# Kernel tuning notes

Hardware: AMD Instinct MI355X
Metric: run time of the kernel (lower is better)

## Reference

```python
import jax, jax.numpy as jnp
import numpy as np

H = 768
HEADS = 12
HD = H // HEADS
INTER = 3072
EPS = 1e-6


def setup_inputs() -> dict:
    key = jax.random.key(0)
    ks = jax.random.split(key, 10)
    B, T = 4, 1024
    scale = 0.02
    return {
        "x": jax.random.normal(ks[0], (B, T, H), jnp.float32),
        "mask": jnp.ones((B, T), jnp.float32),
        "w_qkv": jax.random.normal(ks[1], (H, 3 * H), jnp.float32) * scale,
        "w_o": jax.random.normal(ks[2], (H, H), jnp.float32) * scale,
        "tau": jnp.full((HEADS,), 5.0, jnp.float32),
        "w1": jax.random.normal(ks[3], (H, INTER), jnp.float32) * scale,
        "b1": jnp.zeros((INTER,), jnp.float32),
        "w2": jax.random.normal(ks[4], (INTER, H), jnp.float32) * scale,
        "b2": jnp.zeros((H,), jnp.float32),
        "nb1": jnp.zeros((H,), jnp.float32),
        "nb2": jnp.zeros((H,), jnp.float32),
    }


def _block(x, mask, w_qkv, w_o, tau, w1, b1, w2, b2, nb1, nb2):
    B, T, C = x.shape
    qkv = x @ w_qkv                                  # [B,T,3H]
    q, k, v = jnp.split(qkv, 3, axis=-1)
    q = q.reshape(B, T, HEADS, HD)
    k = k.reshape(B, T, HEADS, HD)
    v = v.reshape(B, T, HEADS, HD)
    # 2quad attention: quadratic-normalized scores instead of softmax
    s = jnp.einsum("bthd,bshd->bhts", q, k) / jnp.sqrt(jnp.float32(HD))
    s = s / tau[None, :, None, None]
    w = s * s                                        # [B,HEADS,T,T]
    w = w * mask[:, None, None, :]                   # zero masked keys
    w = w / (jnp.sum(w, axis=-1, keepdims=True) + EPS)
    out = jnp.einsum("bhts,bshd->bthd", w, v).reshape(B, T, C)
    out = out @ w_o
    x = x + 0.2 * out + nb1                          # scaled residual + bias-only norm1
    ffn = jax.nn.relu(x @ w1 + b1) @ w2 + b2
    x = x + ffn + nb2                                # residual + bias-only norm2
    return x


def reference(x, mask, w_qkv, w_o, tau, w1, b1, w2, b2, nb1, nb2):
    return _block(x, mask, w_qkv, w_o, tau, w1, b1, w2, b2, nb1, nb2)
```

## Files before the change

### kernel.cpp

```cpp
#include <hip/hip_runtime.h>

typedef __bf16 bf16x8 __attribute__((ext_vector_type(8)));
typedef float f32x4 __attribute__((ext_vector_type(4)));
typedef unsigned short u16;
typedef unsigned long long u64;

#define HDIM 768
#define NHEADS 12
#define SEQ 1024
#define NBATCH 4
#define ROWS 4096
#define QKV3 2304
#define INTERDIM 3072

__device__ __forceinline__ u16 f2bf(float f) {
  union { float f; unsigned int u; } v; v.f = f;
  unsigned int r = v.u + 0x7fffu + ((v.u >> 16) & 1u);
  return (u16)(r >> 16);
}

__device__ __forceinline__ void gload16(const u16* g, u16* l) {
  __builtin_amdgcn_global_load_lds(
      (const __attribute__((address_space(1))) void*)g,
      (__attribute__((address_space(3))) void*)l, 16, 0, 0);
}

__device__ __forceinline__ unsigned ldsoff(const void* p) {
  return (unsigned)(unsigned long long)(const __attribute__((address_space(3))) char*)p;
}

__device__ __forceinline__ u64 tr8(unsigned a) {
  u64 r;
  asm volatile("ds_read_b64_tr_b16 %0, %1" : "=v"(r) : "v"(a));
  return r;
}

union B8 { u64 q[2]; bf16x8 v; };

__global__ __launch_bounds__(256) void k_prep(
    const float* __restrict__ x, u16* __restrict__ xb,
    const float* __restrict__ wqkv, u16* __restrict__ wqkvT,
    const float* __restrict__ wo, u16* __restrict__ woT,
    const float* __restrict__ w1, u16* __restrict__ w1T,
    const float* __restrict__ w2, u16* __restrict__ w2T) {
  __shared__ float tile[32][33];
  int bid = blockIdx.x, tid = threadIdx.x;
  if (bid < 3072) {
    int i = bid * 256 + tid;
    float4 f = reinterpret_cast<const float4*>(x)[i];
    ushort4 o;
    o.x = f2bf(f.x); o.y = f2bf(f.y); o.z = f2bf(f.z); o.w = f2bf(f.w);
    reinterpret_cast<ushort4*>(xb)[i] = o;
    return;
  }
  const float* in; u16* outp; int K, N, t;
  if (bid < 4800)      { in = wqkv; outp = wqkvT; K = 768;  N = 2304; t = bid - 3072; }
  else if (bid < 5376) { in = wo;   outp = woT;   K = 768;  N = 768;  t = bid - 4800; }
  else if (bid < 7680) { in = w1;   outp = w1T;   K = 768;  N = 3072; t = bid - 5376; }
  else                 { in = w2;   outp = w2T;   K = 3072; N = 768;  t = bid - 7680; }
  int ntx = N >> 5;
  int bx = t % ntx, by = t / ntx;
  int tx = tid & 31, ty = tid >> 5;
  int n0 = bx * 32, k0 = by * 32;
#pragma unroll
  for (int i = 0; i < 32; i += 8)
    tile[ty + i][tx] = in[(size_t)(k0 + ty + i) * N + n0 + tx];
  __syncthreads();
#pragma unroll
  for (int i = 0; i < 32; i += 8)
    outp[(size_t)(n0 + ty + i) * K + k0 + tx] = f2bf(tile[tx][ty + i]);
}

template<int BN, int MODE>
__global__ __launch_bounds__(256) void k_gemm(
    const u16* __restrict__ A, const u16* __restrict__ Bt,
    int M, int N, int K, int ksplit,
    u16* __restrict__ obf, float* __restrict__ of32,
    const float* __restrict__ e1, const float* __restrict__ e2) {
  constexpr int BM = 128, BK = 64;
  constexpr int WC = (BN == 128) ? 2 : 1;
  constexpr int WR = 4 / WC;
  constexpr int WM = BM / WR;
  constexpr int WN = BN / WC;
  constexpr int MFR = WM / 16;
  constexpr int NFR = WN / 16;
  constexpr int AISS = BM / 32;
  constexpr int BISS = BN / 32;
  __shared__ u16 As[BM * BK];
  __shared__ u16 Bs[BN * BK];
  int tid = threadIdx.x, lane = tid & 63, wid = tid >> 6;
  int wr = wid / WC, wc = wid % WC;

  int gx = gridDim.x;
  int nwg = gx * gridDim.y;
  int orig = blockIdx.y * gx + blockIdx.x;
  int cpx = nwg >> 3;
  int swz = (orig & 7) * cpx + (orig >> 3);
  int bx = swz % gx, by = swz / gx;

  int m0 = by * BM, n0 = bx * BN;
  int Kc = K / ksplit, k0 = blockIdx.z * Kc;
  int fr = lane & 15, fg = lane >> 4, fk = fg * 8;

  f32x4 acc[MFR][NFR] = {};

  int r = tid >> 3;
  int cswz = ((tid & 7) * 8) ^ ((r & 3) << 4);
  const u16* Ag = A + (size_t)(m0 + r) * K + k0 + cswz;
  const u16* Bg = Bt + (size_t)(n0 + r) * K + k0 + cswz;
  u16* Asl = &As[wid * 512];
  u16* Bsl = &Bs[wid * 512];

  for (int kt = 0; kt < Kc; kt += BK) {
    __syncthreads();
#pragma unroll
    for (int i = 0; i < AISS; i++)
      gload16(Ag + kt + (size_t)(i * 32) * K, Asl + i * 2048);
#pragma unroll
    for (int i = 0; i < BISS; i++)
      gload16(Bg + kt + (size_t)(i * 32) * K, Bsl + i * 2048);
    __syncthreads();

#pragma unroll
    for (int kk = 0; kk < 2; kk++) {
      bf16x8 af[MFR], bfv[NFR];
#pragma unroll
      for (int mi = 0; mi < MFR; mi++) {
        int row = wr * WM + mi * 16 + fr;
        int ce = (kk * 32 + fk) ^ ((row & 3) << 4);
        af[mi] = *reinterpret_cast<const bf16x8*>(&As[row * BK + ce]);
      }
#pragma unroll
      for (int ni = 0; ni < NFR; ni++) {
        int row = wc * WN + ni * 16 + fr;
        int ce = (kk * 32 + fk) ^ ((row & 3) << 4);
        bfv[ni] = *reinterpret_cast<const bf16x8*>(&Bs[row * BK + ce]);
      }
#pragma unroll
      for (int mi = 0; mi < MFR; mi++)
#pragma unroll
        for (int ni = 0; ni < NFR; ni++)
          acc[mi][ni] = __builtin_amdgcn_mfma_f32_16x16x32_bf16(af[mi], bfv[ni], acc[mi][ni], 0, 0, 0);
    }
  }

  float* part = (MODE == 3) ? of32 + (size_t)blockIdx.z * ((size_t)M * N) : of32;
#pragma unroll
  for (int mi = 0; mi < MFR; mi++) {
#pragma unroll
    for (int ni = 0; ni < NFR; ni++) {
#pragma unroll
      for (int i = 0; i < 4; i++) {
        int row = m0 + wr * WM + mi * 16 + fg * 4 + i;
        int col = n0 + wc * WN + ni * 16 + fr;
        float v = acc[mi][ni][i];
        size_t idx = (size_t)row * N + col;
        if constexpr (MODE == 0) {
          obf[idx] = f2bf(v);
        } else if constexpr (MODE == 1) {
          float t = e1[idx] + 0.2f * v + e2[col];
          of32[idx] = t;
          obf[idx] = f2bf(t);
        } else if constexpr (MODE == 2) {
          float t = v + e1[col];
          t = t > 0.f ? t : 0.f;
          obf[idx] = f2bf(t);
        } else {
          part[idx] = v;
        }
      }
    }
  }
}

__global__ void k_ffn2_reduce(const float* __restrict__ p, const float* __restrict__ x1f,
                              const float* __restrict__ b2, const float* __restrict__ nb2,
                              float* __restrict__ out) {
  int i = blockIdx.x * 256 + threadIdx.x;
  int col4 = (i * 4) % HDIM;
  float4 s = reinterpret_cast<const float4*>(x1f)[i];
  float4 bb = *reinterpret_cast<const float4*>(b2 + col4);
  float4 nn = *reinterpret_cast<const float4*>(nb2 + col4);
  s.x += bb.x + nn.x; s.y += bb.y + nn.y; s.z += bb.z + nn.z; s.w += bb.w + nn.w;
#pragma unroll
  for (int z = 0; z < 2; z++) {
    float4 pv = reinterpret_cast<const float4*>(p + (size_t)z * ROWS * HDIM)[i];
    s.x += pv.x; s.y += pv.y; s.z += pv.z; s.w += pv.w;
  }
  reinterpret_cast<float4*>(out)[i] = s;
}

__global__ __launch_bounds__(512) void k_attn(
    const u16* __restrict__ qkv, const float* __restrict__ mask,
    const float* __restrict__ tau, u16* __restrict__ outp) {
  __shared__ u16 Ks[64 * 72];
  __shared__ u16 Vs[64 * 64];
  __shared__ u16 Ps[8 * 1024];
  int tid = threadIdx.x, lane = tid & 63, w = tid >> 6;
  int h = blockIdx.y, b = blockIdx.z;
  int fr = lane & 15, fg = lane >> 4, fk = fg * 8;
  int rb = b * SEQ;
  float rs = 1.0f / (8.0f * tau[h]);
  float rs2 = rs * rs;

  int t0 = blockIdx.x * 128 + w * 16;
  const u16* qrow = qkv + (size_t)(rb + t0 + fr) * QKV3 + h * 64;
  bf16x8 aq0 = *reinterpret_cast<const bf16x8*>(qrow + fk);
  bf16x8 aq1 = *reinterpret_cast<const bf16x8*>(qrow + 32 + fk);

  f32x4 acco[4] = {};
  f32x4 accd = {};

  int sr = tid >> 3, c = tid & 7;
  const u16* kg = qkv + (size_t)(rb + sr) * QKV3 + HDIM + h * 64 + c * 8;
  const u16* vg = kg + HDIM;
  u16* kw = &Ks[sr * 72 + c * 8];
  u16* vw = &Vs[((sr >> 2) * 4 + (c >> 1)) * 64 + (sr & 3) * 16 + (c & 1) * 8];
  unsigned psb = ldsoff(&Ps[w * 1024]);
  unsigned vsb = ldsoff(Vs);

  __bf16 onev = (__bf16)1.0f;
  bf16x8 ones = {onev, onev, onev, onev, onev, onev, onev, onev};

  int4 kreg = *reinterpret_cast<const int4*>(kg);
  int4 vreg = *reinterpret_cast<const int4*>(vg);

  for (int st = 0; st < SEQ; st += 64) {
    __syncthreads();
    *reinterpret_cast<int4*>(kw) = kreg;
    *reinterpret_cast<int4*>(vw) = vreg;
    __syncthreads();
    if (st + 64 < SEQ) {
      kreg = *reinterpret_cast<const int4*>(kg + (size_t)(st + 64) * QKV3);
      vreg = *reinterpret_cast<const int4*>(vg + (size_t)(st + 64) * QKV3);
    }

#pragma unroll
    for (int sf = 0; sf < 4; sf++) {
      bf16x8 bk0 = *reinterpret_cast<const bf16x8*>(&Ks[(sf * 16 + fr) * 72 + fk]);
      bf16x8 bk1 = *reinterpret_cast<const bf16x8*>(&Ks[(sf * 16 + fr) * 72 + 32 + fk]);
      f32x4 s = {};
      s = __builtin_amdgcn_mfma_f32_16x16x32_bf16(aq0, bk0, s, 0, 0, 0);
      s = __builtin_amdgcn_mfma_f32_16x16x32_bf16(aq1, bk1, s, 0, 0, 0);
      float rm = rs2 * mask[b * SEQ + st + sf * 16 + fr];
      u64 pw = 0;
#pragma unroll
      for (int i = 0; i < 4; i++) {
        float wv = s[i] * s[i] * rm;
        pw |= (u64)f2bf(wv) << (16 * i);
      }
      *reinterpret_cast<u64*>(&Ps[w * 1024 + (sf * 4 + (fr >> 2)) * 64 + (fr & 3) * 16 + fg * 4]) = pw;
    }
    asm volatile("s_waitcnt lgkmcnt(0)" ::: "memory");
    __builtin_amdgcn_sched_barrier(0);

    u64 pa0 = tr8(psb + (fg * 2 + 0) * 128 + fr * 2);
    u64 pa1 = tr8(psb + (fg * 2 + 1) * 128 + fr * 2);
    u64 pa2 = tr8(psb + (8 + fg * 2 + 0) * 128 + fr * 2);
    u64 pa3 = tr8(psb + (8 + fg * 2 + 1) * 128 + fr * 2);
    u64 vb[4][4];
#pragma unroll
    for (int df = 0; df < 4; df++) {
      vb[df][0] = tr8(vsb + ((fg * 2 + 0) * 4 + df) * 128 + fr * 2);
      vb[df][1] = tr8(vsb + ((fg * 2 + 1) * 4 + df) * 128 + fr * 2);
      vb[df][2] = tr8(vsb + ((8 + fg * 2 + 0) * 4 + df) * 128 + fr * 2);
      vb[df][3] = tr8(vsb + ((8 + fg * 2 + 1) * 4 + df) * 128 + fr * 2);
    }
    asm volatile("s_waitcnt lgkmcnt(0)" ::: "memory");
    __builtin_amdgcn_sched_barrier(0);

    B8 ap0, ap1;
    ap0.q[0] = pa0; ap0.q[1] = pa1;
    ap1.q[0] = pa2; ap1.q[1] = pa3;
#pragma unroll
    for (int df = 0; df < 4; df++) {
      B8 b0, b1;
      b0.q[0] = vb[df][0]; b0.q[1] = vb[df][1];
      b1.q[0] = vb[df][2]; b1.q[1] = vb[df][3];
      acco[df] = __builtin_amdgcn_mfma_f32_16x16x32_bf16(ap0.v, b0.v, acco[df], 0, 0, 0);
      acco[df] = __builtin_amdgcn_mfma_f32_16x16x32_bf16(ap1.v, b1.v, acco[df], 0, 0, 0);
    }
    accd = __builtin_amdgcn_mfma_f32_16x16x32_bf16(ap0.v, ones, accd, 0, 0, 0);
    accd = __builtin_amdgcn_mfma_f32_16x16x32_bf16(ap1.v, ones, accd, 0, 0, 0);
  }

#pragma unroll
  for (int df = 0; df < 4; df++)
#pragma unroll
    for (int i = 0; i < 4; i++) {
      int t = t0 + fg * 4 + i;
      int col = h * 64 + df * 16 + fr;
      float o = acco[df][i] / (accd[i] + 1e-6f);
      outp[(size_t)(rb + t) * HDIM + col] = f2bf(o);
    }
}

extern "C" void kernel_launch(void* const* d_in, const int* in_sizes, int n_in,
                              void* d_out, int out_size, void* d_ws, size_t ws_size,
                              hipStream_t stream) {
  const float* x     = (const float*)d_in[0];
  const float* mask  = (const float*)d_in[1];
  const float* w_qkv = (const float*)d_in[2];
  const float* w_o   = (const float*)d_in[3];
  const float* tau   = (const float*)d_in[4];
  const float* w1    = (const float*)d_in[5];
  const float* b1    = (const float*)d_in[6];
  const float* w2    = (const float*)d_in[7];
  const float* b2    = (const float*)d_in[8];
  const float* nb1   = (const float*)d_in[9];
  const float* nb2   = (const float*)d_in[10];
  float* out = (float*)d_out;
  (void)ws_size; (void)in_sizes; (void)n_in; (void)out_size;

  char* base = (char*)d_ws;
  float* part = (float*)base;
  u16* xb    = (u16*)(base);
  u16* wqkvT = (u16*)(base + 6291456);
  u16* woT   = (u16*)(base + 9830400);
  u16* w1T   = (u16*)(base + 11010048);
  u16* qkvb  = (u16*)(base + 15728640);
  u16* attnb = (u16*)(base + 34603008);
  u16* x1b   = (u16*)(base + 40894464);
  u16* w2T   = (u16*)(base + 50331648);
  float* x1f = (float*)(base + 55050240);
  u16* hb    = (u16*)(base + 67633152);

  k_prep<<<9984, 256, 0, stream>>>(x, xb, w_qkv, wqkvT, w_o, woT, w1, w1T, w2, w2T);

  k_gemm<128, 0><<<dim3(QKV3 / 128, ROWS / 128), 256, 0, stream>>>(
      xb, wqkvT, ROWS, QKV3, HDIM, 1, qkvb, nullptr, nullptr, nullptr);
  k_attn<<<dim3(SEQ / 128, NHEADS, NBATCH), 512, 0, stream>>>(qkvb, mask, tau, attnb);
  k_gemm<64, 1><<<dim3(HDIM / 64, ROWS / 128), 256, 0, stream>>>(
      attnb, woT, ROWS, HDIM, HDIM, 1, x1b, x1f, x, nb1);
  k_gemm<128, 2><<<dim3(INTERDIM / 128, ROWS / 128), 256, 0, stream>>>(
      x1b, w1T, ROWS, INTERDIM, HDIM, 1, hb, nullptr, b1, nullptr);
  k_gemm<64, 3><<<dim3(HDIM / 64, ROWS / 128, 2), 256, 0, stream>>>(
      hb, w2T, ROWS, HDIM, INTERDIM, 2, nullptr, part, nullptr, nullptr);
  k_ffn2_reduce<<<ROWS * HDIM / 4 / 256, 256, 0, stream>>>(part, x1f, b2, nb2, out);
}
```

Before: 164.6 us.

## Use 256x256 double-buffered 8-wave GEMM with split-K 4 for FFN2

Replaces the 128-wide GEMM for the QKV, FFN1 and FFN2 projections with a 256x256-tile, 512-thread kernel. It double-buffers LDS, prefetches the next A and B k-tiles between MFMA phases, and raises wave priority during MFMA bursts. The aim is more data reuse per tile and overlap of global loads with matrix math. FFN2 moves to split-K 4 with a wider partial reduction, and the output projection keeps a dedicated 128x64 kernel. The trade-off is far fewer workgroups than the 256 CUs (144–192 blocks), large LDS use (128KB per block), more partial-sum traffic, and a larger workspace overlapping earlier buffers.

```diff
diff --git a/kernel.cpp b/kernel.cpp
--- a/kernel.cpp
+++ b/kernel.cpp
@@ -71,103 +71,236 @@
     outp[(size_t)(n0 + ty + i) * K + k0 + tx] = f2bf(tile[tx][ty + i]);
 }
 
-template<int BN, int MODE>
-__global__ __launch_bounds__(256) void k_gemm(
+template<int MODE>
+__global__ __launch_bounds__(512, 2) void k_gemm256(
     const u16* __restrict__ A, const u16* __restrict__ Bt,
     int M, int N, int K, int ksplit,
     u16* __restrict__ obf, float* __restrict__ of32,
-    const float* __restrict__ e1, const float* __restrict__ e2) {
-  constexpr int BM = 128, BK = 64;
-  constexpr int WC = (BN == 128) ? 2 : 1;
-  constexpr int WR = 4 / WC;
-  constexpr int WM = BM / WR;
-  constexpr int WN = BN / WC;
-  constexpr int MFR = WM / 16;
-  constexpr int NFR = WN / 16;
-  constexpr int AISS = BM / 32;
-  constexpr int BISS = BN / 32;
-  __shared__ u16 As[BM * BK];
-  __shared__ u16 Bs[BN * BK];
+    const float* __restrict__ e1) {
+  __shared__ u16 lds[2][2][256 * 64];
   int tid = threadIdx.x, lane = tid & 63, wid = tid >> 6;
-  int wr = wid / WC, wc = wid % WC;
+  int wr = wid >> 2, wc = wid & 3;
+  int fr = lane & 15, fg = lane >> 4, fk = fg * 8;
 
   int gx = gridDim.x;
   int nwg = gx * gridDim.y;
   int orig = blockIdx.y * gx + blockIdx.x;
-  int cpx = nwg >> 3;
-  int swz = (orig & 7) * cpx + (orig >> 3);
+  int swz = (orig & 7) * (nwg >> 3) + (orig >> 3);
   int bx = swz % gx, by = swz / gx;
-
-  int m0 = by * BM, n0 = bx * BN;
+  int m0 = by * 256, n0 = bx * 256;
   int Kc = K / ksplit, k0 = blockIdx.z * Kc;
-  int fr = lane & 15, fg = lane >> 4, fk = fg * 8;
-
-  f32x4 acc[MFR][NFR] = {};
+
+  f32x4 acc[8][4] = {};
 
   int r = tid >> 3;
   int cswz = ((tid & 7) * 8) ^ ((r & 3) << 4);
   const u16* Ag = A + (size_t)(m0 + r) * K + k0 + cswz;
   const u16* Bg = Bt + (size_t)(n0 + r) * K + k0 + cswz;
-  u16* Asl = &As[wid * 512];
-  u16* Bsl = &Bs[wid * 512];
-
-  for (int kt = 0; kt < Kc; kt += BK) {
-    __syncthreads();
-#pragma unroll
-    for (int i = 0; i < AISS; i++)
-      gload16(Ag + kt + (size_t)(i * 32) * K, Asl + i * 2048);
-#pragma unroll
-    for (int i = 0; i < BISS; i++)
-      gload16(Bg + kt + (size_t)(i * 32) * K, Bsl + i * 2048);
-    __syncthreads();
-
-#pragma unroll
-    for (int kk = 0; kk < 2; kk++) {
-      bf16x8 af[MFR], bfv[NFR];
-#pragma unroll
-      for (int mi = 0; mi < MFR; mi++) {
-        int row = wr * WM + mi * 16 + fr;
-        int ce = (kk * 32 + fk) ^ ((row & 3) << 4);
-        af[mi] = *reinterpret_cast<const bf16x8*>(&As[row * BK + ce]);
-      }
-#pragma unroll
-      for (int ni = 0; ni < NFR; ni++) {
-        int row = wc * WN + ni * 16 + fr;
-        int ce = (kk * 32 + fk) ^ ((row & 3) << 4);
-        bfv[ni] = *reinterpret_cast<const bf16x8*>(&Bs[row * BK + ce]);
-      }
-#pragma unroll
-      for (int mi = 0; mi < MFR; mi++)
-#pragma unroll
-        for (int ni = 0; ni < NFR; ni++)
-          acc[mi][ni] = __builtin_amdgcn_mfma_f32_16x16x32_bf16(af[mi], bfv[ni], acc[mi][ni], 0, 0, 0);
-    }
-  }
+
+#define STAGE_A(buf, kt) do {                                        \
+    u16* d_ = &lds[buf][0][wid * 512];                               \
+    _Pragma("unroll")                                                \
+    for (int i_ = 0; i_ < 4; i_++)                                   \
+      gload16(Ag + (kt) + (size_t)(i_ * 64) * K, d_ + i_ * 4096);    \
+  } while (0)
+#define STAGE_B(buf, kt) do {                                        \
+    u16* d_ = &lds[buf][1][wid * 512];                               \
+    _Pragma("unroll")                                                \
+    for (int i_ = 0; i_ < 4; i_++)                                   \
+      gload16(Bg + (kt) + (size_t)(i_ * 64) * K, d_ + i_ * 4096);    \
+  } while (0)
+
+  int sw = (fr & 3) << 4;
+  int ce0 = fk ^ sw, ce1 = (32 + fk) ^ sw;
+
+  STAGE_A(0, 0);
+  STAGE_B(0, 0);
+  asm volatile("s_waitcnt vmcnt(0)" ::: "memory");
+  __builtin_amdgcn_s_barrier();
+
+  int nt = Kc / 64;
+  bf16x8 af[4][2], bv0[2][2], bv1[2][2];
+  for (int t = 0; t < nt; t++) {
+    int cur = t & 1;
+    const u16* Ab = &lds[cur][0][0];
+    const u16* Bb = &lds[cur][1][0];
+    bool pf = (t + 1 < nt);
+
+    if (pf) STAGE_A(cur ^ 1, (t + 1) * 64);
+#pragma unroll
+    for (int im = 0; im < 4; im++) {
+      int row = wr * 128 + im * 16 + fr;
+      af[im][0] = *reinterpret_cast<const bf16x8*>(&Ab[row * 64 + ce0]);
+      af[im][1] = *reinterpret_cast<const bf16x8*>(&Ab[row * 64 + ce1]);
+    }
+#pragma unroll
+    for (int in = 0; in < 2; in++) {
+      int row = wc * 64 + in * 16 + fr;
+      bv0[in][0] = *reinterpret_cast<const bf16x8*>(&Bb[row * 64 + ce0]);
+      bv0[in][1] = *reinterpret_cast<const bf16x8*>(&Bb[row * 64 + ce1]);
+    }
+    __builtin_amdgcn_s_barrier();
+    __builtin_amdgcn_s_setprio(1);
+#pragma unroll
+    for (int im = 0; im < 4; im++)
+#pragma unroll
+      for (int in = 0; in < 2; in++)
+#pragma unroll
+        for (int kk = 0; kk < 2; kk++)
+          acc[im][in] = __builtin_amdgcn_mfma_f32_16x16x32_bf16(af[im][kk], bv0[in][kk], acc[im][in], 0, 0, 0);
+    __builtin_amdgcn_s_setprio(0);
+    __builtin_amdgcn_s_barrier();
+
+    if (pf) STAGE_B(cur ^ 1, (t + 1) * 64);
+#pragma unroll
+    for (int in = 0; in < 2; in++) {
+      int row = wc * 64 + (2 + in) * 16 + fr;
+      bv1[in][0] = *reinterpret_cast<const bf16x8*>(&Bb[row * 64 + ce0]);
+      bv1[in][1] = *reinterpret_cast<const bf16x8*>(&Bb[row * 64 + ce1]);
+    }
+    __builtin_amdgcn_s_barrier();
+    __builtin_amdgcn_s_setprio(1);
+#pragma unroll
+    for (int im = 0; im < 4; im++)
+#pragma unroll
+      for (int in = 0; in < 2; in++)
+#pragma unroll
+        for (int kk = 0; kk < 2; kk++)
+          acc[im][2 + in] = __builtin_amdgcn_mfma_f32_16x16x32_bf16(af[im][kk], bv1[in][kk], acc[im][2 + in], 0, 0, 0);
+    __builtin_amdgcn_s_setprio(0);
+    __builtin_amdgcn_s_barrier();
+
+#pragma unroll
+    for (int im = 0; im < 4; im++) {
+      int row = wr * 128 + (4 + im) * 16 + fr;
+      af[im][0] = *reinterpret_cast<const bf16x8*>(&Ab[row * 64 + ce0]);
+      af[im][1] = *reinterpret_cast<const bf16x8*>(&Ab[row * 64 + ce1]);
+    }
+    __builtin_amdgcn_s_barrier();
+    __builtin_amdgcn_s_setprio(1);
+#pragma unroll
+    for (int im = 0; im < 4; im++)
+#pragma unroll
+      for (int in = 0; in < 2; in++)
+#pragma unroll
+        for (int kk = 0; kk < 2; kk++)
+          acc[4 + im][in] = __builtin_amdgcn_mfma_f32_16x16x32_bf16(af[im][kk], bv0[in][kk], acc[4 + im][in], 0, 0, 0);
+    __builtin_amdgcn_s_setprio(0);
+    __builtin_amdgcn_s_barrier();
+
+    __builtin_amdgcn_s_setprio(1);
+#pragma unroll
+    for (int im = 0; im < 4; im++)
+#pragma unroll
+      for (int in = 0; in < 2; in++)
+#pragma unroll
+        for (int kk = 0; kk < 2; kk++)
+          acc[4 + im][2 + in] = __builtin_amdgcn_mfma_f32_16x16x32_bf16(af[im][kk], bv1[in][kk], acc[4 + im][2 + in], 0, 0, 0);
+    __builtin_amdgcn_s_setprio(0);
+    if (pf) {
+      asm volatile("s_waitcnt vmcnt(0)" ::: "memory");
+      __builtin_amdgcn_s_barrier();
+    }
+  }
+#undef STAGE_A
+#undef STAGE_B
 
   float* part = (MODE == 3) ? of32 + (size_t)blockIdx.z * ((size_t)M * N) : of32;
 #pragma unroll
-  for (int mi = 0; mi < MFR; mi++) {
-#pragma unroll
-    for (int ni = 0; ni < NFR; ni++) {
+  for (int mi = 0; mi < 8; mi++) {
+#pragma unroll
+    for (int ni = 0; ni < 4; ni++) {
 #pragma unroll
       for (int i = 0; i < 4; i++) {
-        int row = m0 + wr * WM + mi * 16 + fg * 4 + i;
-        int col = n0 + wc * WN + ni * 16 + fr;
+        int row = m0 + wr * 128 + mi * 16 + fg * 4 + i;
+        int col = n0 + wc * 64 + ni * 16 + fr;
         float v = acc[mi][ni][i];
         size_t idx = (size_t)row * N + col;
         if constexpr (MODE == 0) {
           obf[idx] = f2bf(v);
-        } else if constexpr (MODE == 1) {
-          float t = e1[idx] + 0.2f * v + e2[col];
-          of32[idx] = t;
-          obf[idx] = f2bf(t);
         } else if constexpr (MODE == 2) {
-          float t = v + e1[col];
-          t = t > 0.f ? t : 0.f;
-          obf[idx] = f2bf(t);
+          float tv = v + e1[col];
+          obf[idx] = f2bf(tv > 0.f ? tv : 0.f);
         } else {
           part[idx] = v;
         }
+      }
+    }
+  }
+}
+
+__global__ __launch_bounds__(256) void k_gemm_wo(
+    const u16* __restrict__ A, const u16* __restrict__ Bt,
+    int M, int N, int K,
+    u16* __restrict__ obf, float* __restrict__ of32,
+    const float* __restrict__ e1, const float* __restrict__ e2) {
+  constexpr int BM = 128, BN = 64, BK = 64;
+  __shared__ u16 As[BM * BK];
+  __shared__ u16 Bs[BN * BK];
+  int tid = threadIdx.x, lane = tid & 63, wid = tid >> 6;
+  int wr = wid;
+  int gx = gridDim.x;
+  int nwg = gx * gridDim.y;
+  int orig = blockIdx.y * gx + blockIdx.x;
+  int swz = (orig & 7) * (nwg >> 3) + (orig >> 3);
+  int bx = swz % gx, by = swz / gx;
+  int m0 = by * BM, n0 = bx * BN;
+  int fr = lane & 15, fg = lane >> 4, fk = fg * 8;
+
+  f32x4 acc[2][4] = {};
+
+  int r = tid >> 3;
+  int cswz = ((tid & 7) * 8) ^ ((r & 3) << 4);
+  const u16* Ag = A + (size_t)(m0 + r) * K + cswz;
+  const u16* Bg = Bt + (size_t)(n0 + r) * K + cswz;
+  u16* Asl = &As[wid * 512];
+  u16* Bsl = &Bs[wid * 512];
+
+  for (int kt = 0; kt < K; kt += BK) {
+    __syncthreads();
+#pragma unroll
+    for (int i = 0; i < 4; i++)
+      gload16(Ag + kt + (size_t)(i * 32) * K, Asl + i * 2048);
+#pragma unroll
+    for (int i = 0; i < 2; i++)
+      gload16(Bg + kt + (size_t)(i * 32) * K, Bsl + i * 2048);
+    __syncthreads();
+
+#pragma unroll
+    for (int kk = 0; kk < 2; kk++) {
+      bf16x8 af[2], bfv[4];
+#pragma unroll
+      for (int mi = 0; mi < 2; mi++) {
+        int row = wr * 32 + mi * 16 + fr;
+        int ce = (kk * 32 + fk) ^ ((row & 3) << 4);
+        af[mi] = *reinterpret_cast<const bf16x8*>(&As[row * BK + ce]);
+      }
+#pragma unroll
+      for (int ni = 0; ni < 4; ni++) {
+        int row = ni * 16 + fr;
+        int ce = (kk * 32 + fk) ^ ((row & 3) << 4);
+        bfv[ni] = *reinterpret_cast<const bf16x8*>(&Bs[row * BK + ce]);
+      }
+#pragma unroll
+      for (int mi = 0; mi < 2; mi++)
+#pragma unroll
+        for (int ni = 0; ni < 4; ni++)
+          acc[mi][ni] = __builtin_amdgcn_mfma_f32_16x16x32_bf16(af[mi], bfv[ni], acc[mi][ni], 0, 0, 0);
+    }
+  }
+
+#pragma unroll
+  for (int mi = 0; mi < 2; mi++) {
+#pragma unroll
+    for (int ni = 0; ni < 4; ni++) {
+#pragma unroll
+      for (int i = 0; i < 4; i++) {
+        int row = m0 + wr * 32 + mi * 16 + fg * 4 + i;
+        int col = n0 + ni * 16 + fr;
+        size_t idx = (size_t)row * N + col;
+        float t = e1[idx] + 0.2f * acc[mi][ni][i] + e2[col];
+        of32[idx] = t;
+        obf[idx] = f2bf(t);
       }
     }
   }
@@ -183,7 +316,7 @@
   float4 nn = *reinterpret_cast<const float4*>(nb2 + col4);
   s.x += bb.x + nn.x; s.y += bb.y + nn.y; s.z += bb.z + nn.z; s.w += bb.w + nn.w;
 #pragma unroll
-  for (int z = 0; z < 2; z++) {
+  for (int z = 0; z < 4; z++) {
     float4 pv = reinterpret_cast<const float4*>(p + (size_t)z * ROWS * HDIM)[i];
     s.x += pv.x; s.y += pv.y; s.z += pv.z; s.w += pv.w;
   }
@@ -327,14 +460,14 @@
 
   k_prep<<<9984, 256, 0, stream>>>(x, xb, w_qkv, wqkvT, w_o, woT, w1, w1T, w2, w2T);
 
-  k_gemm<128, 0><<<dim3(QKV3 / 128, ROWS / 128), 256, 0, stream>>>(
-      xb, wqkvT, ROWS, QKV3, HDIM, 1, qkvb, nullptr, nullptr, nullptr);
+  k_gemm256<0><<<dim3(QKV3 / 256, ROWS / 256), 512, 0, stream>>>(
+      xb, wqkvT, ROWS, QKV3, HDIM, 1, qkvb, nullptr, nullptr);
   k_attn<<<dim3(SEQ / 128, NHEADS, NBATCH), 512, 0, stream>>>(qkvb, mask, tau, attnb);
-  k_gemm<64, 1><<<dim3(HDIM / 64, ROWS / 128), 256, 0, stream>>>(
-      attnb, woT, ROWS, HDIM, HDIM, 1, x1b, x1f, x, nb1);
-  k_gemm<128, 2><<<dim3(INTERDIM / 128, ROWS / 128), 256, 0, stream>>>(
-      x1b, w1T, ROWS, INTERDIM, HDIM, 1, hb, nullptr, b1, nullptr);
-  k_gemm<64, 3><<<dim3(HDIM / 64, ROWS / 128, 2), 256, 0, stream>>>(
-      hb, w2T, ROWS, HDIM, INTERDIM, 2, nullptr, part, nullptr, nullptr);
+  k_gemm_wo<<<dim3(HDIM / 64, ROWS / 128), 256, 0, stream>>>(
+      attnb, woT, ROWS, HDIM, HDIM, x1b, x1f, x, nb1);
+  k_gemm256<2><<<dim3(INTERDIM / 256, ROWS / 256), 512, 0, stream>>>(
+      x1b, w1T, ROWS, INTERDIM, HDIM, 1, hb, nullptr, b1);
+  k_gemm256<3><<<dim3(HDIM / 256, ROWS / 256, 4), 512, 0, stream>>>(
+      hb, w2T, ROWS, HDIM, INTERDIM, 4, nullptr, part, nullptr);
   k_ffn2_reduce<<<ROWS * HDIM / 4 / 256, 256, 0, stream>>>(part, x1f, b2, nb2, out);
 }
```

New measurement: 173.5 us, median of 4. +5.4%, slower.

## Double-buffer GEMM LDS tiles with async prefetch and widen FFN2 tile

Applied to the files above, without the earlier changes.

Reworks the shared GEMM kernel into a two-stage software pipeline. BK drops to 32, A/B tiles are double-buffered in LDS, and loads for step t+2 are issued while MFMAs run on the current buffer, gated by explicit vmcnt/lgkmcnt waits and barriers plus s_setprio around the MFMA block. The goal is to hide global-to-LDS load latency that the previous load-sync-compute loop exposed. The FFN2 split-K GEMM also switches to BN=128 tiles, giving fewer, larger blocks. Risks are the hand-tuned vmcnt counts being wrong for a given BISS and halving the work done per barrier.

```diff
diff --git a/kernel.cpp b/kernel.cpp
--- a/kernel.cpp
+++ b/kernel.cpp
@@ -77,72 +77,80 @@
     int M, int N, int K, int ksplit,
     u16* __restrict__ obf, float* __restrict__ of32,
     const float* __restrict__ e1, const float* __restrict__ e2) {
-  constexpr int BM = 128, BK = 64;
+  constexpr int BM = 128, BK = 32;
   constexpr int WC = (BN == 128) ? 2 : 1;
   constexpr int WR = 4 / WC;
   constexpr int WM = BM / WR;
   constexpr int WN = BN / WC;
   constexpr int MFR = WM / 16;
   constexpr int NFR = WN / 16;
-  constexpr int AISS = BM / 32;
-  constexpr int BISS = BN / 32;
-  __shared__ u16 As[BM * BK];
-  __shared__ u16 Bs[BN * BK];
+  constexpr int BISS = BN / 64;
+  __shared__ u16 As[2][BM * BK];
+  __shared__ u16 Bs[2][BN * BK];
   int tid = threadIdx.x, lane = tid & 63, wid = tid >> 6;
   int wr = wid / WC, wc = wid % WC;
+  int fr = lane & 15, fg = lane >> 4, fk = fg * 8;
 
   int gx = gridDim.x;
   int nwg = gx * gridDim.y;
   int orig = blockIdx.y * gx + blockIdx.x;
-  int cpx = nwg >> 3;
-  int swz = (orig & 7) * cpx + (orig >> 3);
+  int swz = (orig & 7) * (nwg >> 3) + (orig >> 3);
   int bx = swz % gx, by = swz / gx;
-
   int m0 = by * BM, n0 = bx * BN;
   int Kc = K / ksplit, k0 = blockIdx.z * Kc;
-  int fr = lane & 15, fg = lane >> 4, fk = fg * 8;
 
   f32x4 acc[MFR][NFR] = {};
 
-  int r = tid >> 3;
-  int cswz = ((tid & 7) * 8) ^ ((r & 3) << 4);
+  int r = tid >> 2;
+  int cswz = ((tid & 3) * 8) ^ (((r >> 1) & 3) << 3);
   const u16* Ag = A + (size_t)(m0 + r) * K + k0 + cswz;
   const u16* Bg = Bt + (size_t)(n0 + r) * K + k0 + cswz;
-  u16* Asl = &As[wid * 512];
-  u16* Bsl = &Bs[wid * 512];
-
-  for (int kt = 0; kt < Kc; kt += BK) {
-    __syncthreads();
-#pragma unroll
-    for (int i = 0; i < AISS; i++)
-      gload16(Ag + kt + (size_t)(i * 32) * K, Asl + i * 2048);
-#pragma unroll
-    for (int i = 0; i < BISS; i++)
-      gload16(Bg + kt + (size_t)(i * 32) * K, Bsl + i * 2048);
-    __syncthreads();
-
-#pragma unroll
-    for (int kk = 0; kk < 2; kk++) {
-      bf16x8 af[MFR], bfv[NFR];
-#pragma unroll
-      for (int mi = 0; mi < MFR; mi++) {
-        int row = wr * WM + mi * 16 + fr;
-        int ce = (kk * 32 + fk) ^ ((row & 3) << 4);
-        af[mi] = *reinterpret_cast<const bf16x8*>(&As[row * BK + ce]);
-      }
-#pragma unroll
-      for (int ni = 0; ni < NFR; ni++) {
-        int row = wc * WN + ni * 16 + fr;
-        int ce = (kk * 32 + fk) ^ ((row & 3) << 4);
-        bfv[ni] = *reinterpret_cast<const bf16x8*>(&Bs[row * BK + ce]);
-      }
-#pragma unroll
-      for (int mi = 0; mi < MFR; mi++)
-#pragma unroll
-        for (int ni = 0; ni < NFR; ni++)
-          acc[mi][ni] = __builtin_amdgcn_mfma_f32_16x16x32_bf16(af[mi], bfv[ni], acc[mi][ni], 0, 0, 0);
-    }
-  }
+
+#define STAGE(t2) do {                                                   \
+    int b_ = (t2) & 1; int kt_ = (t2) * BK;                              \
+    gload16(Ag + kt_, &As[b_][wid * 512]);                               \
+    gload16(Ag + kt_ + (size_t)64 * K, &As[b_][2048 + wid * 512]);       \
+    gload16(Bg + kt_, &Bs[b_][wid * 512]);                               \
+    if constexpr (BISS == 2)                                             \
+      gload16(Bg + kt_ + (size_t)64 * K, &Bs[b_][2048 + wid * 512]);     \
+  } while (0)
+
+  int ce = fk ^ (((fr >> 1) & 3) << 3);
+
+  int nt = Kc / BK;
+  STAGE(0);
+  STAGE(1);
+
+  for (int t = 0; t < nt; t++) {
+    int cur = t & 1;
+    if (t == nt - 1) {
+      asm volatile("s_waitcnt vmcnt(0)\n\ts_barrier" ::: "memory");
+    } else if constexpr (BISS == 2) {
+      asm volatile("s_waitcnt vmcnt(4)\n\ts_barrier" ::: "memory");
+    } else {
+      asm volatile("s_waitcnt vmcnt(3)\n\ts_barrier" ::: "memory");
+    }
+
+    bf16x8 af[MFR], bv[NFR];
+#pragma unroll
+    for (int mi = 0; mi < MFR; mi++)
+      af[mi] = *reinterpret_cast<const bf16x8*>(&As[cur][(wr * WM + mi * 16 + fr) * BK + ce]);
+#pragma unroll
+    for (int ni = 0; ni < NFR; ni++)
+      bv[ni] = *reinterpret_cast<const bf16x8*>(&Bs[cur][(wc * WN + ni * 16 + fr) * BK + ce]);
+
+    asm volatile("s_waitcnt lgkmcnt(0)\n\ts_barrier" ::: "memory");
+    if (t + 2 < nt) STAGE(t + 2);
+
+    __builtin_amdgcn_s_setprio(1);
+#pragma unroll
+    for (int mi = 0; mi < MFR; mi++)
+#pragma unroll
+      for (int ni = 0; ni < NFR; ni++)
+        acc[mi][ni] = __builtin_amdgcn_mfma_f32_16x16x32_bf16(af[mi], bv[ni], acc[mi][ni], 0, 0, 0);
+    __builtin_amdgcn_s_setprio(0);
+  }
+#undef STAGE
 
   float* part = (MODE == 3) ? of32 + (size_t)blockIdx.z * ((size_t)M * N) : of32;
 #pragma unroll
@@ -163,8 +171,7 @@
           obf[idx] = f2bf(t);
         } else if constexpr (MODE == 2) {
           float t = v + e1[col];
-          t = t > 0.f ? t : 0.f;
-          obf[idx] = f2bf(t);
+          obf[idx] = f2bf(t > 0.f ? t : 0.f);
         } else {
           part[idx] = v;
         }
@@ -334,7 +341,7 @@
       attnb, woT, ROWS, HDIM, HDIM, 1, x1b, x1f, x, nb1);
   k_gemm<128, 2><<<dim3(INTERDIM / 128, ROWS / 128), 256, 0, stream>>>(
       x1b, w1T, ROWS, INTERDIM, HDIM, 1, hb, nullptr, b1, nullptr);
-  k_gemm<64, 3><<<dim3(HDIM / 64, ROWS / 128, 2), 256, 0, stream>>>(
+  k_gemm<128, 3><<<dim3(HDIM / 128, ROWS / 128, 2), 256, 0, stream>>>(
       hb, w2T, ROWS, HDIM, INTERDIM, 2, nullptr, part, nullptr, nullptr);
   k_ffn2_reduce<<<ROWS * HDIM / 4 / 256, 256, 0, stream>>>(part, x1f, b2, nb2, out);
 }
```

Result: no change. 167.4 us (+1.7%).
